# Kernel optimization log

Measured on AMD Instinct MI355X. Metric: run time of the kernel, lower is better.

## Reference

```python
import jax, jax.numpy as jnp
import numpy as np

N = 512  # hardcoded in the CUDA kernel via #define N 512
PACKED_LEN = N * (N + 1) // 2  # 131328


def _unpack_upper(p):
    """Unpack row-major packed upper-triangular storage into a dense [N,N] matrix.

    Packed index of element (i, j), j >= i:  i*(2N - i + 1)//2 + (j - i).
    Lower triangle is zero.
    """
    i = jnp.arange(N)[:, None]
    j = jnp.arange(N)[None, :]
    mask = j >= i
    pidx = (i * (2 * N - i + 1)) // 2 + (j - i)
    pidx = jnp.where(mask, pidx, 0)  # clamp invalid indices to a safe value
    return jnp.where(mask, p[pidx], jnp.zeros((), p.dtype))


def setup_inputs() -> dict:
    key = jax.random.key(0)
    kA, kB = jax.random.split(key)
    A = jax.random.normal(kA, (PACKED_LEN,), dtype=jnp.float32)
    B = jax.random.normal(kB, (PACKED_LEN,), dtype=jnp.float32)
    return {"A": A, "B": B}


def reference(A, B):
    # C[i,j] = sum_{k=i}^{j} A[i,k] * B[k,j] for j >= i, else 0.
    # Product of two upper-triangular matrices is upper-triangular, so a dense
    # matmul of the unpacked matrices reproduces the kernel's output exactly
    # (lower-triangle entries are structurally zero).
    Au = _unpack_upper(A)  # [N, N]
    Bu = _unpack_upper(B)  # [N, N]
    return Au @ Bu  # [N, N]
```

## Files before the change

kernel.cpp:

```cpp
#include <hip/hip_runtime.h>

#define NN 512

__global__ __launch_bounds__(256) void ut_fused(const float* __restrict__ A,
                                                const float* __restrict__ B,
                                                float* __restrict__ C) {
    const int jt   = (int)blockIdx.x;
    const int rb   = (int)blockIdx.y;
    const int w    = (int)threadIdx.x >> 6;
    const int lane = (int)threadIdx.x & 63;
    const int i0   = rb << 2;
    const int it   = i0 >> 6;
    const int j    = (jt << 6) + lane;

    if (jt < it) {
        C[(i0 + w) * NN + j] = 0.0f;
        return;
    }

    __shared__ float red[4][4][64];

    const float* pA[4];
    #pragma unroll
    for (int r = 0; r < 4; ++r) {
        const int ir = i0 + r;
        pA[r] = A + (((ir * (2 * NN - ir + 1)) >> 1) - ir);
    }

    const int kbeg = i0;
    const int kend = (jt + 1) << 6;
    const int L    = (kend - kbeg) >> 2;
    const int k0   = kbeg + w * L;
    const int k1   = k0 + L;

    int idxB = ((k0 * (2 * NN - k0 + 1)) >> 1) + (j - k0);

    float acc0 = 0.f, acc1 = 0.f, acc2 = 0.f, acc3 = 0.f;
    #pragma unroll 4
    for (int k = k0; k < k1; ++k) {
        const float bv = (k <= j) ? B[idxB] : 0.0f;
        const float a0 = (k >= i0)     ? pA[0][k] : 0.0f;
        const float a1 = (k >= i0 + 1) ? pA[1][k] : 0.0f;
        const float a2 = (k >= i0 + 2) ? pA[2][k] : 0.0f;
        const float a3 = (k >= i0 + 3) ? pA[3][k] : 0.0f;
        acc0 += a0 * bv;
        acc1 += a1 * bv;
        acc2 += a2 * bv;
        acc3 += a3 * bv;
        idxB += NN - 1 - k;
    }

    red[w][0][lane] = acc0;
    red[w][1][lane] = acc1;
    red[w][2][lane] = acc2;
    red[w][3][lane] = acc3;
    __syncthreads();

    const float s = (red[0][w][lane] + red[1][w][lane]) +
                    (red[2][w][lane] + red[3][w][lane]);
    C[(i0 + w) * NN + j] = s;
}

extern "C" void kernel_launch(void* const* d_in, const int* in_sizes, int n_in,
                              void* d_out, int out_size, void* d_ws, size_t ws_size,
                              hipStream_t stream) {
    const float* A = (const float*)d_in[0];
    const float* B = (const float*)d_in[1];
    float* C = (float*)d_out;
    ut_fused<<<dim3(8, 128), dim3(256), 0, stream>>>(A, B, C);
}
```

Baseline: 24.30 us.

## Widen row band to eight rows per block and split k-loop by region

Each block now computes eight output rows instead of four, using 512 threads with eight warps splitting the k range. Every B element loaded is reused across eight A rows, halving B traffic per output. The k loop for off-diagonal tiles is split into a triangular head, a branch-free interior and a masked tail, which removes per-iteration predicates in the common case. The cost is more registers per thread and fewer, larger blocks, plus a larger shared reduction buffer.

After: 22.54 us. -7.2%, faster.

```diff
diff --git a/kernel.cpp b/kernel.cpp
--- a/kernel.cpp
+++ b/kernel.cpp
@@ -2,15 +2,15 @@
 
 #define NN 512
 
-__global__ __launch_bounds__(256) void ut_fused(const float* __restrict__ A,
-                                                const float* __restrict__ B,
-                                                float* __restrict__ C) {
+__global__ __launch_bounds__(512) void ut_fused8(const float* __restrict__ A,
+                                                 const float* __restrict__ B,
+                                                 float* __restrict__ C) {
     const int jt   = (int)blockIdx.x;
-    const int rb   = (int)blockIdx.y;
+    const int band = (int)blockIdx.y;
     const int w    = (int)threadIdx.x >> 6;
     const int lane = (int)threadIdx.x & 63;
-    const int i0   = rb << 2;
-    const int it   = i0 >> 6;
+    const int i0   = band << 3;
+    const int it   = band >> 3;
     const int j    = (jt << 6) + lane;
 
     if (jt < it) {
@@ -18,46 +18,72 @@
         return;
     }
 
-    __shared__ float red[4][4][64];
+    __shared__ float red[8][8][64];
 
-    const float* pA[4];
+    const float* pA[8];
     #pragma unroll
-    for (int r = 0; r < 4; ++r) {
+    for (int r = 0; r < 8; ++r) {
         const int ir = i0 + r;
         pA[r] = A + (((ir * (2 * NN - ir + 1)) >> 1) - ir);
     }
 
-    const int kbeg = i0;
     const int kend = (jt + 1) << 6;
-    const int L    = (kend - kbeg) >> 2;
-    const int k0   = kbeg + w * L;
+    const int L    = (kend - i0) >> 3;
+    const int k0   = i0 + w * L;
     const int k1   = k0 + L;
 
     int idxB = ((k0 * (2 * NN - k0 + 1)) >> 1) + (j - k0);
 
-    float acc0 = 0.f, acc1 = 0.f, acc2 = 0.f, acc3 = 0.f;
-    #pragma unroll 4
-    for (int k = k0; k < k1; ++k) {
-        const float bv = (k <= j) ? B[idxB] : 0.0f;
-        const float a0 = (k >= i0)     ? pA[0][k] : 0.0f;
-        const float a1 = (k >= i0 + 1) ? pA[1][k] : 0.0f;
-        const float a2 = (k >= i0 + 2) ? pA[2][k] : 0.0f;
-        const float a3 = (k >= i0 + 3) ? pA[3][k] : 0.0f;
-        acc0 += a0 * bv;
-        acc1 += a1 * bv;
-        acc2 += a2 * bv;
-        acc3 += a3 * bv;
-        idxB += NN - 1 - k;
+    float acc[8];
+    #pragma unroll
+    for (int r = 0; r < 8; ++r) acc[r] = 0.f;
+
+    int k = k0;
+    if (jt == it) {
+        for (; k < k1; ++k) {
+            const float bv = (k <= j) ? B[idxB] : 0.f;
+            #pragma unroll
+            for (int r = 0; r < 8; ++r) {
+                const float av = (k >= i0 + r) ? pA[r][k] : 0.f;
+                acc[r] += av * bv;
+            }
+            idxB += NN - 1 - k;
+        }
+    } else {
+        const int kaE = (k1 < i0 + 8) ? k1 : (i0 + 8);
+        for (; k < kaE; ++k) {
+            const float bv = B[idxB];
+            #pragma unroll
+            for (int r = 0; r < 8; ++r) {
+                const float av = (k >= i0 + r) ? pA[r][k] : 0.f;
+                acc[r] += av * bv;
+            }
+            idxB += NN - 1 - k;
+        }
+        const int jtd = jt << 6;
+        const int kiE = (k1 < jtd) ? k1 : jtd;
+        #pragma unroll 8
+        for (; k < kiE; ++k) {
+            const float bv = B[idxB];
+            #pragma unroll
+            for (int r = 0; r < 8; ++r) acc[r] += pA[r][k] * bv;
+            idxB += NN - 1 - k;
+        }
+        for (; k < k1; ++k) {
+            const float bv = (k <= j) ? B[idxB] : 0.f;
+            #pragma unroll
+            for (int r = 0; r < 8; ++r) acc[r] += pA[r][k] * bv;
+            idxB += NN - 1 - k;
+        }
     }
 
-    red[w][0][lane] = acc0;
-    red[w][1][lane] = acc1;
-    red[w][2][lane] = acc2;
-    red[w][3][lane] = acc3;
+    #pragma unroll
+    for (int r = 0; r < 8; ++r) red[w][r][lane] = acc[r];
     __syncthreads();
 
-    const float s = (red[0][w][lane] + red[1][w][lane]) +
-                    (red[2][w][lane] + red[3][w][lane]);
+    float s = 0.f;
+    #pragma unroll
+    for (int t = 0; t < 8; ++t) s += red[t][w][lane];
     C[(i0 + w) * NN + j] = s;
 }
 
@@ -67,5 +93,5 @@
     const float* A = (const float*)d_in[0];
     const float* B = (const float*)d_in[1];
     float* C = (float*)d_out;
-    ut_fused<<<dim3(8, 128), dim3(256), 0, stream>>>(A, B, C);
+    ut_fused8<<<dim3(8, 64), dim3(512), 0, stream>>>(A, B, C);
 }
```
